# Kernel optimization log

Measured on AMD Instinct MI355X. Metric: run time of the kernel, lower is better.

The kernel has to match this reference:

```python
import jax, jax.numpy as jnp
import numpy as np

NUM_HEADS = 12


def setup_inputs() -> dict:
    key = jax.random.key(0)
    ks = jax.random.split(key, 8)
    B, Nq, Nk, C = 4, 2048, 2048, 768
    s = 0.02
    return {
        "query": jax.random.normal(ks[0], (B, Nq, C), dtype=jnp.float32),
        "key": jax.random.normal(ks[1], (B, Nk, C), dtype=jnp.float32),
        "value": jax.random.normal(ks[2], (B, Nk, C), dtype=jnp.float32),
        "Wq": jax.random.normal(ks[3], (C, C), dtype=jnp.float32) * s,
        "Wk": jax.random.normal(ks[4], (C, C), dtype=jnp.float32) * s,
        "Wv": jax.random.normal(ks[5], (C, C), dtype=jnp.float32) * s,
        "Wo": jax.random.normal(ks[6], (C, C), dtype=jnp.float32) * s,
        "bo": jnp.zeros((C,), dtype=jnp.float32),
    }


def reference(query, key, value, Wq, Wk, Wv, Wo, bo):
    B, Nq, C = query.shape
    Nk = key.shape[1]
    H = NUM_HEADS
    Dh = C // H
    scale = Dh ** -0.5
    # nn.Linear: x @ W.T ; split heads -> [B, H, N, Dh]
    q = (query @ Wq.T).reshape(B, Nq, H, Dh).transpose(0, 2, 1, 3)
    k = (key @ Wk.T).reshape(B, Nk, H, Dh).transpose(0, 2, 1, 3)
    v = (value @ Wv.T).reshape(B, Nk, H, Dh).transpose(0, 2, 1, 3)
    # attention logits [B, H, Nq, Nk]
    attn = jnp.einsum("bhqd,bhkd->bhqk", q, k) * scale
    attn = jax.nn.softmax(attn, axis=-1)
    x = jnp.einsum("bhqk,bhkd->bhqd", attn, v)  # [B, H, Nq, Dh]
    x = x.transpose(0, 2, 1, 3).reshape(B, Nq, C)
    return x @ Wo.T + bo
```

## Files before the change

### kernel.cpp

```cpp
#include <hip/hip_runtime.h>
#include <hip/hip_bf16.h>
#include <stdint.h>

typedef unsigned short u16;
typedef unsigned int   u32;
typedef unsigned long long u64;

typedef __attribute__((ext_vector_type(8)))  short short8;
typedef __attribute__((ext_vector_type(4)))  u32   u32x4;
typedef __attribute__((ext_vector_type(4)))  float f32x4;
typedef __attribute__((ext_vector_type(16))) float f32x16;


__device__ __forceinline__ u16 f2bf(float f) {
  u32 u = __builtin_bit_cast(u32, f);
  u += 0x7FFFu + ((u >> 16) & 1u);
  return (u16)(u >> 16);
}

__device__ __forceinline__ void gload16(const void* g, void* l) {
  __builtin_amdgcn_global_load_lds((__attribute__((address_space(1))) void*)(g),
                                   (__attribute__((address_space(3))) void*)(l),
                                   16, 0, 0);
}

__device__ __forceinline__ u32 cvtpk(float lo, float hi) {
  u32 r;
  asm("v_cvt_pk_bf16_f32 %0, %1, %2" : "=v"(r) : "v"(lo), "v"(hi));
  return r;
}


__global__ __launch_bounds__(256)
void cvt3_kernel(const float* __restrict__ a, const float* __restrict__ b,
                 const float* __restrict__ c, u16* __restrict__ oa,
                 u16* __restrict__ ob, u16* __restrict__ oc, int n4) {
  int i = blockIdx.x * 256 + threadIdx.x;
  if (i >= n4) return;
  const float* in = blockIdx.y == 0 ? a : blockIdx.y == 1 ? b : c;
  u16* out = blockIdx.y == 0 ? oa : blockIdx.y == 1 ? ob : oc;
  float4 v = reinterpret_cast<const float4*>(in)[i];
  u64 pk = (u64)f2bf(v.x) | ((u64)f2bf(v.y) << 16)
         | ((u64)f2bf(v.z) << 32) | ((u64)f2bf(v.w) << 48);
  reinterpret_cast<u64*>(out)[i] = pk;
}

__global__ __launch_bounds__(256)
void cvtw_kernel(const float* __restrict__ Wq, const float* __restrict__ Wk,
                 const float* __restrict__ Wv, const float* __restrict__ Wo,
                 u16* __restrict__ Wcat, u16* __restrict__ WoB, int n4, float qs) {
  int i = blockIdx.x * 256 + threadIdx.x;
  if (i >= n4) return;
  int y = blockIdx.y;
  const float* in = y == 0 ? Wq : y == 1 ? Wk : y == 2 ? Wv : Wo;
  u16* out = y == 0 ? Wcat : y == 1 ? (Wcat + 589824) : y == 2 ? (Wcat + 1179648) : WoB;
  float s = y == 0 ? qs : 1.f;
  float4 v = reinterpret_cast<const float4*>(in)[i];
  u64 pk = (u64)f2bf(v.x * s) | ((u64)f2bf(v.y * s) << 16)
         | ((u64)f2bf(v.z * s) << 32) | ((u64)f2bf(v.w * s) << 48);
  reinterpret_cast<u64*>(out)[i] = pk;
}

template<int MODE>
__global__ __launch_bounds__(256)
void gemm128(const u16* __restrict__ Aq, const u16* __restrict__ Ak,
             const u16* __restrict__ Av, const u16* __restrict__ Bw,
             u16* __restrict__ Cqk, u16* __restrict__ Vt,
             float* __restrict__ Cout, const float* __restrict__ bias) {
  constexpr int K  = 768;
  constexpr int KT = K / 32;
  constexpr int NBN = (MODE == 0) ? 18 : 6;
  __shared__ char lds[32768];
  char* A0 = lds;          char* A1 = lds + 8192;
  char* B0 = lds + 16384;  char* B1 = lds + 24576;

  const int tid = threadIdx.x, lane = tid & 63, wid = tid >> 6;
  const int hw = blockIdx.x;
  const int L = (hw & 7) * (64 * NBN / 8) + (hw >> 3);
  const int bm = L / NBN, bn = L - bm * NBN;
  const int wr = wid >> 1, wc = wid & 1;

  const u16* Abase = Aq;
  if constexpr (MODE == 0) Abase = (bn < 6) ? Aq : (bn < 12) ? Ak : Av;

  const char* Ag = (const char*)Abase + (size_t)bm * 128 * (K * 2);
  const char* Bg = (const char*)Bw    + (size_t)bn * 128 * (K * 2);

  f32x4 acc[4][4];
  #pragma unroll
  for (int m = 0; m < 4; ++m)
    #pragma unroll
    for (int n = 0; n < 4; ++n)
      #pragma unroll
      for (int r = 0; r < 4; ++r) acc[m][n][r] = 0.f;

  #pragma unroll
  for (int c = 0; c < 2; ++c) {
    int chunk = c * 4 + wid;
    int off = chunk * 1024 + lane * 16;
    int row = off >> 6, colb = off & 63;
    gload16(Ag + (size_t)row * (K * 2) + colb, A0 + chunk * 1024);
    gload16(Bg + (size_t)row * (K * 2) + colb, B0 + chunk * 1024);
  }
  __syncthreads();

  for (int kt = 0; kt < KT; ++kt) {
    const int cur = kt & 1;
    char* Ac = cur ? A1 : A0;  char* Bc = cur ? B1 : B0;
    char* An = cur ? A0 : A1;  char* Bn = cur ? B0 : B1;
    if (kt + 1 < KT) {
      #pragma unroll
      for (int c = 0; c < 2; ++c) {
        int chunk = c * 4 + wid;
        int off = chunk * 1024 + lane * 16;
        int row = off >> 6, colb = off & 63;
        gload16(Ag + (size_t)row * (K * 2) + (kt + 1) * 64 + colb, An + chunk * 1024);
        gload16(Bg + (size_t)row * (K * 2) + (kt + 1) * 64 + colb, Bn + chunk * 1024);
      }
    }
    short8 af[4], bf[4];
    #pragma unroll
    for (int m = 0; m < 4; ++m) {
      int row = wr * 64 + m * 16 + (lane & 15);
      af[m] = *reinterpret_cast<const short8*>(Ac + row * 64 + ((lane >> 4) * 16));
    }
    #pragma unroll
    for (int n = 0; n < 4; ++n) {
      int row = wc * 64 + n * 16 + (lane & 15);
      bf[n] = *reinterpret_cast<const short8*>(Bc + row * 64 + ((lane >> 4) * 16));
    }
    #pragma unroll
    for (int m = 0; m < 4; ++m)
      #pragma unroll
      for (int n = 0; n < 4; ++n)
        acc[m][n] = __builtin_amdgcn_mfma_f32_16x16x32_bf16(af[m], bf[n], acc[m][n], 0, 0, 0);
    __syncthreads();
  }

  if constexpr (MODE == 0) {
    if (bn < 12) {
      #pragma unroll
      for (int m = 0; m < 4; ++m) {
        int grow0 = bm * 128 + wr * 64 + m * 16 + ((lane >> 4) << 2);
        #pragma unroll
        for (int n = 0; n < 4; ++n) {
          int col = bn * 128 + wc * 64 + n * 16 + (lane & 15);
          #pragma unroll
          for (int r = 0; r < 4; ++r)
            Cqk[(size_t)(grow0 + r) * 1536 + col] = f2bf(acc[m][n][r]);
        }
      }
    } else {
      #pragma unroll
      for (int m = 0; m < 4; ++m) {
        int grow0 = bm * 128 + wr * 64 + m * 16 + ((lane >> 4) << 2);
        int bb = grow0 >> 11, nn = grow0 & 2047;
        #pragma unroll
        for (int n = 0; n < 4; ++n) {
          int vc = (bn - 12) * 128 + wc * 64 + n * 16 + (lane & 15);
          int hid = vc >> 6, d = vc & 63;
          u64 pk = (u64)f2bf(acc[m][n][0]) | ((u64)f2bf(acc[m][n][1]) << 16)
                 | ((u64)f2bf(acc[m][n][2]) << 32) | ((u64)f2bf(acc[m][n][3]) << 48);
          *reinterpret_cast<u64*>(Vt + ((size_t)(bb * 12 + hid) * 64 + d) * 2048 + nn) = pk;
        }
      }
    }
  } else {
    #pragma unroll
    for (int m = 0; m < 4; ++m) {
      int grow0 = bm * 128 + wr * 64 + m * 16 + ((lane >> 4) << 2);
      #pragma unroll
      for (int n = 0; n < 4; ++n) {
        int col = bn * 128 + wc * 64 + n * 16 + (lane & 15);
        float bs = bias[col];
        #pragma unroll
        for (int r = 0; r < 4; ++r)
          Cout[(size_t)(grow0 + r) * 768 + col] = acc[m][n][r] + bs;
      }
    }
  }
}

__global__ __launch_bounds__(256)
void attn_fwd(const u16* __restrict__ QK, const u16* __restrict__ Vt,
              u16* __restrict__ X) {
  __shared__ char lds[32768];
  char* K0 = lds;          char* K1 = lds + 8192;
  char* V0 = lds + 16384;  char* V1 = lds + 24576;

  const int tid = threadIdx.x, lane = tid & 63, wid = tid >> 6;
  const int hw = blockIdx.x;
  const int L = (hw & 7) * 96 + (hw >> 3);
  const int bh = L >> 4, qt = L & 15;
  const int b = bh / 12, h = bh - b * 12;
  const int hh = lane >> 5;

  const char* Qg = (const char*)QK + ((size_t)(b * 2048 + qt * 128) * 1536 + h * 64) * 2;
  const char* Kg = (const char*)QK + ((size_t)(b * 2048) * 1536 + 768 + h * 64) * 2;
  const char* Vg = (const char*)Vt + ((size_t)bh * 64 * 2048) * 2;

  const int off0 = wid * 1024 + lane * 16;
  const int off1 = off0 + 4096;
  const int r0 = off0 >> 7, i0 = (off0 & 127) ^ ((r0 & 7) << 4);
  const int r1 = off1 >> 7, i1 = (off1 & 127) ^ ((r1 & 7) << 4);
  const int pb0 = (r0 >> 2) & 7, pb1 = (r1 >> 2) & 7;
  const int kr0 = (r0 & 32) | ((((pb0 & 1) << 1) | ((pb0 >> 1) & 1) | (pb0 & 4)) << 2) | (r0 & 3);
  const int kr1 = (r1 & 32) | ((((pb1 & 1) << 1) | ((pb1 >> 1) & 1) | (pb1 & 4)) << 2) | (r1 & 3);
  const size_t kso0 = (size_t)kr0 * 3072 + i0, kso1 = (size_t)kr1 * 3072 + i1;
  const size_t vso0 = (size_t)r0 * 4096 + i0, vso1 = (size_t)r1 * 4096 + i1;

  gload16(Kg + kso0, K0 + off0);
  gload16(Kg + kso1, K0 + off1);
  gload16(Vg + vso0, V0 + off0);
  gload16(Vg + vso1, V0 + off1);

  short8 qf[4];
  {
    const char* Qrow = Qg + (size_t)(wid * 32 + (lane & 31)) * 3072 + hh * 16;
    #pragma unroll
    for (int kk = 0; kk < 4; ++kk)
      qf[kk] = *reinterpret_cast<const short8*>(Qrow + kk * 32);
  }
  __syncthreads();

  f32x16 o0, o1;
  #pragma unroll
  for (int r = 0; r < 16; ++r) { o0[r] = 0.f; o1[r] = 0.f; }
  float l_run = 0.f;

  for (int t = 0; t < 32; ++t) {
    const int cur = t & 1;
    char* Kc = cur ? K1 : K0;  char* Vc = cur ? V1 : V0;
    char* Kn = cur ? K0 : K1;  char* Vn = cur ? V0 : V1;
    if (t + 1 < 32) {
      const char* Kgn = Kg + (size_t)(t + 1) * 64 * 3072;
      const char* Vgn = Vg + (size_t)(t + 1) * 128;
      gload16(Kgn + kso0, Kn + off0);
      gload16(Kgn + kso1, Kn + off1);
      gload16(Vgn + vso0, Vn + off0);
      gload16(Vgn + vso1, Vn + off1);
    }

    f32x16 sa, sb;
    #pragma unroll
    for (int r = 0; r < 16; ++r) { sa[r] = 0.f; sb[r] = 0.f; }
    {
      const int ra = lane & 31;
      const int swa = (ra & 7) << 4;
      const char* Ka = Kc + ra * 128;
      const char* Kb2 = Kc + (32 + ra) * 128;
      __builtin_amdgcn_s_setprio(1);
      #pragma unroll
      for (int kk = 0; kk < 4; ++kk) {
        int inner = (kk * 32 + hh * 16) ^ swa;
        short8 ka = *reinterpret_cast<const short8*>(Ka + inner);
        short8 kb = *reinterpret_cast<const short8*>(Kb2 + inner);
        sa = __builtin_amdgcn_mfma_f32_32x32x16_bf16(ka, qf[kk], sa, 0, 0, 0);
        sb = __builtin_amdgcn_mfma_f32_32x32x16_bf16(kb, qf[kk], sb, 0, 0, 0);
      }
      __builtin_amdgcn_s_setprio(0);
    }

    float pa[16], pb[16];
    float s0 = 0.f, s1 = 0.f, s2 = 0.f, s3 = 0.f;
    #pragma unroll
    for (int r = 0; r < 16; r += 4) {
      pa[r]     = __builtin_amdgcn_exp2f(sa[r]);     s0 += pa[r];
      pa[r + 1] = __builtin_amdgcn_exp2f(sa[r + 1]); s1 += pa[r + 1];
      pa[r + 2] = __builtin_amdgcn_exp2f(sa[r + 2]); s2 += pa[r + 2];
      pa[r + 3] = __builtin_amdgcn_exp2f(sa[r + 3]); s3 += pa[r + 3];
    }
    #pragma unroll
    for (int r = 0; r < 16; r += 4) {
      pb[r]     = __builtin_amdgcn_exp2f(sb[r]);     s0 += pb[r];
      pb[r + 1] = __builtin_amdgcn_exp2f(sb[r + 1]); s1 += pb[r + 1];
      pb[r + 2] = __builtin_amdgcn_exp2f(sb[r + 2]); s2 += pb[r + 2];
      pb[r + 3] = __builtin_amdgcn_exp2f(sb[r + 3]); s3 += pb[r + 3];
    }
    l_run += (s0 + s1) + (s2 + s3);

    short8 pf[4];
    {
      u32x4 w0 = { cvtpk(pa[0],  pa[1]),  cvtpk(pa[2],  pa[3]),
                   cvtpk(pa[4],  pa[5]),  cvtpk(pa[6],  pa[7]) };
      u32x4 w1 = { cvtpk(pa[8],  pa[9]),  cvtpk(pa[10], pa[11]),
                   cvtpk(pa[12], pa[13]), cvtpk(pa[14], pa[15]) };
      u32x4 w2 = { cvtpk(pb[0],  pb[1]),  cvtpk(pb[2],  pb[3]),
                   cvtpk(pb[4],  pb[5]),  cvtpk(pb[6],  pb[7]) };
      u32x4 w3 = { cvtpk(pb[8],  pb[9]),  cvtpk(pb[10], pb[11]),
                   cvtpk(pb[12], pb[13]), cvtpk(pb[14], pb[15]) };
      pf[0] = __builtin_bit_cast(short8, w0);
      pf[1] = __builtin_bit_cast(short8, w1);
      pf[2] = __builtin_bit_cast(short8, w2);
      pf[3] = __builtin_bit_cast(short8, w3);
    }

    {
      const int rv = lane & 31;
      const int swv = (rv & 7) << 4;
      const char* Va = Vc + rv * 128;
      const char* Vb = Vc + (32 + rv) * 128;
      __builtin_amdgcn_s_setprio(1);
      #pragma unroll
      for (int st = 0; st < 4; ++st) {
        int inner = (st * 32 + hh * 16) ^ swv;
        short8 v0 = *reinterpret_cast<const short8*>(Va + inner);
        short8 v1 = *reinterpret_cast<const short8*>(Vb + inner);
        o0 = __builtin_amdgcn_mfma_f32_32x32x16_bf16(v0, pf[st], o0, 0, 0, 0);
        o1 = __builtin_amdgcn_mfma_f32_32x32x16_bf16(v1, pf[st], o1, 0, 0, 0);
      }
      __builtin_amdgcn_s_setprio(0);
    }
    __syncthreads();
  }

  l_run += __shfl_xor(l_run, 32);

  const float invl = __builtin_amdgcn_rcpf(l_run);
  const int q = qt * 128 + wid * 32 + (lane & 31);
  u16* Xp = X + (size_t)(b * 2048 + q) * 768;
  #pragma unroll
  for (int mt = 0; mt < 2; ++mt) {
    #pragma unroll
    for (int rr = 0; rr < 4; ++rr) {
      float e0 = (mt ? o1[rr * 4 + 0] : o0[rr * 4 + 0]) * invl;
      float e1 = (mt ? o1[rr * 4 + 1] : o0[rr * 4 + 1]) * invl;
      float e2 = (mt ? o1[rr * 4 + 2] : o0[rr * 4 + 2]) * invl;
      float e3 = (mt ? o1[rr * 4 + 3] : o0[rr * 4 + 3]) * invl;
      int col = h * 64 + mt * 32 + 8 * rr + 4 * hh;
      u64 pk = (u64)f2bf(e0) | ((u64)f2bf(e1) << 16)
             | ((u64)f2bf(e2) << 32) | ((u64)f2bf(e3) << 48);
      *reinterpret_cast<u64*>(Xp + col) = pk;
    }
  }
}


extern "C" void kernel_launch(void* const* d_in, const int* in_sizes, int n_in,
                              void* d_out, int out_size, void* d_ws, size_t ws_size,
                              hipStream_t stream) {
  const float* query = (const float*)d_in[0];
  const float* key   = (const float*)d_in[1];
  const float* value = (const float*)d_in[2];
  const float* Wq    = (const float*)d_in[3];
  const float* Wk    = (const float*)d_in[4];
  const float* Wv    = (const float*)d_in[5];
  const float* Wo    = (const float*)d_in[6];
  const float* bo    = (const float*)d_in[7];

  char* ws = (char*)d_ws;
  u16* Wcat = (u16*)ws;
  u16* WoB  = (u16*)(ws + (size_t)2304 * 768 * 2);
  u16* Xq   = (u16*)(ws + (size_t)2304 * 768 * 2 + (size_t)768 * 768 * 2);
  u16* Xk   = Xq  + (size_t)8192 * 768;
  u16* Xv   = Xk  + (size_t)8192 * 768;
  u16* QKb  = Xv  + (size_t)8192 * 768;
  u16* VtB  = QKb + (size_t)8192 * 1536;

  const float qs = 0.125f * 1.4426950408889634f;
  cvtw_kernel<<<dim3(576, 4), 256, 0, stream>>>(Wq, Wk, Wv, Wo, Wcat, WoB, 147456, qs);
  cvt3_kernel<<<dim3(6144, 3), 256, 0, stream>>>(query, key, value, Xq, Xk, Xv, 1572864);

  gemm128<0><<<dim3(1152), 256, 0, stream>>>(Xq, Xk, Xv, Wcat, QKb, VtB, nullptr, nullptr);
  attn_fwd<<<dim3(768), 256, 0, stream>>>(QKb, VtB, Xq);
  gemm128<1><<<dim3(384), 256, 0, stream>>>(Xq, nullptr, nullptr, WoB, nullptr, nullptr,
                                            (float*)d_out, bo);
}
```

Before: 169.8 us.

## Triple-buffer K/V tiles in attention with prefetch distance two

Moves the attention kernel's K/V staging from double to triple buffering in LDS, issuing global-to-LDS loads two tiles ahead. Full __syncthreads is replaced by explicit vmcnt waits plus s_barrier, so a wave only waits for the oldest outstanding tile. The aim is to hide more global load latency behind MFMA work, at the cost of 48KB of LDS per block, which may reduce occupancy.

```diff
diff --git a/kernel.cpp b/kernel.cpp
--- a/kernel.cpp
+++ b/kernel.cpp
@@ -184,9 +184,9 @@
 __global__ __launch_bounds__(256)
 void attn_fwd(const u16* __restrict__ QK, const u16* __restrict__ Vt,
               u16* __restrict__ X) {
-  __shared__ char lds[32768];
-  char* K0 = lds;          char* K1 = lds + 8192;
-  char* V0 = lds + 16384;  char* V1 = lds + 24576;
+  __shared__ char lds[49152];
+  char* Kb0 = lds;          char* Kb1 = lds + 8192;   char* Kb2 = lds + 16384;
+  char* Vb0 = lds + 24576;  char* Vb1 = lds + 32768;  char* Vb2 = lds + 40960;
 
   const int tid = threadIdx.x, lane = tid & 63, wid = tid >> 6;
   const int hw = blockIdx.x;
@@ -209,10 +209,17 @@
   const size_t kso0 = (size_t)kr0 * 3072 + i0, kso1 = (size_t)kr1 * 3072 + i1;
   const size_t vso0 = (size_t)r0 * 4096 + i0, vso1 = (size_t)r1 * 4096 + i1;
 
-  gload16(Kg + kso0, K0 + off0);
-  gload16(Kg + kso1, K0 + off1);
-  gload16(Vg + vso0, V0 + off0);
-  gload16(Vg + vso1, V0 + off1);
+  auto stage = [&](int t, char* Kd, char* Vd) {
+    const char* Kgn = Kg + (size_t)t * 64 * 3072;
+    const char* Vgn = Vg + (size_t)t * 128;
+    gload16(Kgn + kso0, Kd + off0);
+    gload16(Kgn + kso1, Kd + off1);
+    gload16(Vgn + vso0, Vd + off0);
+    gload16(Vgn + vso1, Vd + off1);
+  };
+
+  stage(0, Kb0, Vb0);
+  stage(1, Kb1, Vb1);
 
   short8 qf[4];
   {
@@ -221,26 +228,15 @@
     for (int kk = 0; kk < 4; ++kk)
       qf[kk] = *reinterpret_cast<const short8*>(Qrow + kk * 32);
   }
-  __syncthreads();
+  asm volatile("s_waitcnt vmcnt(8)" ::: "memory");
+  __builtin_amdgcn_s_barrier();
 
   f32x16 o0, o1;
   #pragma unroll
   for (int r = 0; r < 16; ++r) { o0[r] = 0.f; o1[r] = 0.f; }
   float l_run = 0.f;
 
-  for (int t = 0; t < 32; ++t) {
-    const int cur = t & 1;
-    char* Kc = cur ? K1 : K0;  char* Vc = cur ? V1 : V0;
-    char* Kn = cur ? K0 : K1;  char* Vn = cur ? V0 : V1;
-    if (t + 1 < 32) {
-      const char* Kgn = Kg + (size_t)(t + 1) * 64 * 3072;
-      const char* Vgn = Vg + (size_t)(t + 1) * 128;
-      gload16(Kgn + kso0, Kn + off0);
-      gload16(Kgn + kso1, Kn + off1);
-      gload16(Vgn + vso0, Vn + off0);
-      gload16(Vgn + vso1, Vn + off1);
-    }
-
+  auto tile_body = [&](const char* Kc, const char* Vc) {
     f32x16 sa, sb;
     #pragma unroll
     for (int r = 0; r < 16; ++r) { sa[r] = 0.f; sb[r] = 0.f; }
@@ -248,13 +244,13 @@
       const int ra = lane & 31;
       const int swa = (ra & 7) << 4;
       const char* Ka = Kc + ra * 128;
-      const char* Kb2 = Kc + (32 + ra) * 128;
+      const char* Kb_ = Kc + (32 + ra) * 128;
       __builtin_amdgcn_s_setprio(1);
       #pragma unroll
       for (int kk = 0; kk < 4; ++kk) {
         int inner = (kk * 32 + hh * 16) ^ swa;
         short8 ka = *reinterpret_cast<const short8*>(Ka + inner);
-        short8 kb = *reinterpret_cast<const short8*>(Kb2 + inner);
+        short8 kb = *reinterpret_cast<const short8*>(Kb_ + inner);
         sa = __builtin_amdgcn_mfma_f32_32x32x16_bf16(ka, qf[kk], sa, 0, 0, 0);
         sb = __builtin_amdgcn_mfma_f32_32x32x16_bf16(kb, qf[kk], sb, 0, 0, 0);
       }
@@ -299,20 +295,34 @@
       const int rv = lane & 31;
       const int swv = (rv & 7) << 4;
       const char* Va = Vc + rv * 128;
-      const char* Vb = Vc + (32 + rv) * 128;
+      const char* Vb_ = Vc + (32 + rv) * 128;
       __builtin_amdgcn_s_setprio(1);
       #pragma unroll
       for (int st = 0; st < 4; ++st) {
         int inner = (st * 32 + hh * 16) ^ swv;
         short8 v0 = *reinterpret_cast<const short8*>(Va + inner);
-        short8 v1 = *reinterpret_cast<const short8*>(Vb + inner);
+        short8 v1 = *reinterpret_cast<const short8*>(Vb_ + inner);
         o0 = __builtin_amdgcn_mfma_f32_32x32x16_bf16(v0, pf[st], o0, 0, 0, 0);
         o1 = __builtin_amdgcn_mfma_f32_32x32x16_bf16(v1, pf[st], o1, 0, 0, 0);
       }
       __builtin_amdgcn_s_setprio(0);
     }
-    __syncthreads();
-  }
+  };
+
+  char* Kc = Kb0; char* Kn1 = Kb1; char* Kn2 = Kb2;
+  char* Vc = Vb0; char* Vn1 = Vb1; char* Vn2 = Vb2;
+  for (int t = 0; t < 30; ++t) {
+    stage(t + 2, Kn2, Vn2);
+    tile_body(Kc, Vc);
+    asm volatile("s_waitcnt vmcnt(4)" ::: "memory");
+    __builtin_amdgcn_s_barrier();
+    char* tk = Kc; Kc = Kn1; Kn1 = Kn2; Kn2 = tk;
+    char* tv = Vc; Vc = Vn1; Vn1 = Vn2; Vn2 = tv;
+  }
+  tile_body(Kc, Vc);
+  asm volatile("s_waitcnt vmcnt(0)" ::: "memory");
+  __builtin_amdgcn_s_barrier();
+  tile_body(Kn1, Vn1);
 
   l_run += __shfl_xor(l_run, 32);
 
```

Result: no change. 171.6 us (+1.1%).

## Fuse fp32-to-bf16 activation conversion into QKV projection GEMM loads

Applied to the files above, without the earlier changes.

Removes the separate cvt3 conversion kernel and has the QKV GEMM stream fp32 query/key/value tiles directly into LDS with an XOR swizzle, converting to bf16 in registers before the MFMA. This drops one kernel launch and a full write and read of the bf16 activation copies. In exchange, the A tile doubles in LDS size (48KB for mode 0), doubles global A traffic per GEMM tile, and adds conversion instructions to the inner loop, which may reduce occupancy.

```diff
diff --git a/kernel.cpp b/kernel.cpp
--- a/kernel.cpp
+++ b/kernel.cpp
@@ -30,20 +30,6 @@
   return r;
 }
 
-
-__global__ __launch_bounds__(256)
-void cvt3_kernel(const float* __restrict__ a, const float* __restrict__ b,
-                 const float* __restrict__ c, u16* __restrict__ oa,
-                 u16* __restrict__ ob, u16* __restrict__ oc, int n4) {
-  int i = blockIdx.x * 256 + threadIdx.x;
-  if (i >= n4) return;
-  const float* in = blockIdx.y == 0 ? a : blockIdx.y == 1 ? b : c;
-  u16* out = blockIdx.y == 0 ? oa : blockIdx.y == 1 ? ob : oc;
-  float4 v = reinterpret_cast<const float4*>(in)[i];
-  u64 pk = (u64)f2bf(v.x) | ((u64)f2bf(v.y) << 16)
-         | ((u64)f2bf(v.z) << 32) | ((u64)f2bf(v.w) << 48);
-  reinterpret_cast<u64*>(out)[i] = pk;
-}
 
 __global__ __launch_bounds__(256)
 void cvtw_kernel(const float* __restrict__ Wq, const float* __restrict__ Wk,
@@ -63,16 +49,19 @@
 
 template<int MODE>
 __global__ __launch_bounds__(256)
-void gemm128(const u16* __restrict__ Aq, const u16* __restrict__ Ak,
-             const u16* __restrict__ Av, const u16* __restrict__ Bw,
+void gemm128(const float* __restrict__ Af0, const float* __restrict__ Af1,
+             const float* __restrict__ Af2, const u16* __restrict__ Ab,
+             const u16* __restrict__ Bw,
              u16* __restrict__ Cqk, u16* __restrict__ Vt,
              float* __restrict__ Cout, const float* __restrict__ bias) {
   constexpr int K  = 768;
   constexpr int KT = K / 32;
   constexpr int NBN = (MODE == 0) ? 18 : 6;
-  __shared__ char lds[32768];
-  char* A0 = lds;          char* A1 = lds + 8192;
-  char* B0 = lds + 16384;  char* B1 = lds + 24576;
+  __shared__ char lds[(MODE == 0) ? 49152 : 32768];
+  char* A0 = lds;
+  char* A1 = lds + ((MODE == 0) ? 16384 : 8192);
+  char* B0 = lds + ((MODE == 0) ? 32768 : 16384);
+  char* B1 = B0 + 8192;
 
   const int tid = threadIdx.x, lane = tid & 63, wid = tid >> 6;
   const int hw = blockIdx.x;
@@ -80,11 +69,15 @@
   const int bm = L / NBN, bn = L - bm * NBN;
   const int wr = wid >> 1, wc = wid & 1;
 
-  const u16* Abase = Aq;
-  if constexpr (MODE == 0) Abase = (bn < 6) ? Aq : (bn < 12) ? Ak : Av;
-
-  const char* Ag = (const char*)Abase + (size_t)bm * 128 * (K * 2);
-  const char* Bg = (const char*)Bw    + (size_t)bn * 128 * (K * 2);
+  const char* Agf = nullptr;
+  const char* Ag16 = nullptr;
+  if constexpr (MODE == 0) {
+    const float* Asrc = (bn < 6) ? Af0 : (bn < 12) ? Af1 : Af2;
+    Agf = (const char*)(Asrc + (size_t)bm * 128 * 768);
+  } else {
+    Ag16 = (const char*)Ab + (size_t)bm * 128 * (K * 2);
+  }
+  const char* Bg = (const char*)Bw + (size_t)bn * 128 * (K * 2);
 
   f32x4 acc[4][4];
   #pragma unroll
@@ -94,14 +87,39 @@
       #pragma unroll
       for (int r = 0; r < 4; ++r) acc[m][n][r] = 0.f;
 
-  #pragma unroll
-  for (int c = 0; c < 2; ++c) {
-    int chunk = c * 4 + wid;
-    int off = chunk * 1024 + lane * 16;
-    int row = off >> 6, colb = off & 63;
-    gload16(Ag + (size_t)row * (K * 2) + colb, A0 + chunk * 1024);
-    gload16(Bg + (size_t)row * (K * 2) + colb, B0 + chunk * 1024);
-  }
+  auto stageA32 = [&](char* An, int kt) {
+    if constexpr (MODE == 0) {
+      #pragma unroll
+      for (int j = 0; j < 4; ++j) {
+        int off = j * 4096 + wid * 1024 + lane * 16;
+        int row = off >> 7;
+        int isl = (off & 127) ^ ((row & 7) << 4);
+        gload16(Agf + (size_t)row * 3072 + kt * 128 + isl, An + off);
+      }
+    }
+  };
+  auto stageA16 = [&](char* An, int kt) {
+    if constexpr (MODE == 1) {
+      #pragma unroll
+      for (int c = 0; c < 2; ++c) {
+        int off = (c * 4 + wid) * 1024 + lane * 16;
+        int row = off >> 6, colb = off & 63;
+        gload16(Ag16 + (size_t)row * (K * 2) + kt * 64 + colb, An + off);
+      }
+    }
+  };
+  auto stageB = [&](char* Bn, int kt) {
+    #pragma unroll
+    for (int c = 0; c < 2; ++c) {
+      int off = (c * 4 + wid) * 1024 + lane * 16;
+      int row = off >> 6, colb = off & 63;
+      gload16(Bg + (size_t)row * (K * 2) + kt * 64 + colb, Bn + off);
+    }
+  };
+
+  stageA32(A0, 0);
+  stageA16(A0, 0);
+  stageB(B0, 0);
   __syncthreads();
 
   for (int kt = 0; kt < KT; ++kt) {
@@ -109,20 +127,26 @@
     char* Ac = cur ? A1 : A0;  char* Bc = cur ? B1 : B0;
     char* An = cur ? A0 : A1;  char* Bn = cur ? B0 : B1;
     if (kt + 1 < KT) {
-      #pragma unroll
-      for (int c = 0; c < 2; ++c) {
-        int chunk = c * 4 + wid;
-        int off = chunk * 1024 + lane * 16;
-        int row = off >> 6, colb = off & 63;
-        gload16(Ag + (size_t)row * (K * 2) + (kt + 1) * 64 + colb, An + chunk * 1024);
-        gload16(Bg + (size_t)row * (K * 2) + (kt + 1) * 64 + colb, Bn + chunk * 1024);
-      }
+      stageA32(An, kt + 1);
+      stageA16(An, kt + 1);
+      stageB(Bn, kt + 1);
     }
     short8 af[4], bf[4];
     #pragma unroll
     for (int m = 0; m < 4; ++m) {
       int row = wr * 64 + m * 16 + (lane & 15);
-      af[m] = *reinterpret_cast<const short8*>(Ac + row * 64 + ((lane >> 4) * 16));
+      if constexpr (MODE == 0) {
+        int swz = (row & 7) << 4;
+        int o1 = (lane >> 4) * 32;
+        const char* Ar = Ac + row * 128;
+        f32x4 lo = *reinterpret_cast<const f32x4*>(Ar + (o1 ^ swz));
+        f32x4 hi = *reinterpret_cast<const f32x4*>(Ar + ((o1 + 16) ^ swz));
+        u32x4 pk = { cvtpk(lo[0], lo[1]), cvtpk(lo[2], lo[3]),
+                     cvtpk(hi[0], hi[1]), cvtpk(hi[2], hi[3]) };
+        af[m] = __builtin_bit_cast(short8, pk);
+      } else {
+        af[m] = *reinterpret_cast<const short8*>(Ac + row * 64 + ((lane >> 4) * 16));
+      }
     }
     #pragma unroll
     for (int n = 0; n < 4; ++n) {
@@ -352,17 +376,15 @@
   u16* Wcat = (u16*)ws;
   u16* WoB  = (u16*)(ws + (size_t)2304 * 768 * 2);
   u16* Xq   = (u16*)(ws + (size_t)2304 * 768 * 2 + (size_t)768 * 768 * 2);
-  u16* Xk   = Xq  + (size_t)8192 * 768;
-  u16* Xv   = Xk  + (size_t)8192 * 768;
-  u16* QKb  = Xv  + (size_t)8192 * 768;
+  u16* QKb  = Xq  + (size_t)8192 * 768;
   u16* VtB  = QKb + (size_t)8192 * 1536;
 
   const float qs = 0.125f * 1.4426950408889634f;
   cvtw_kernel<<<dim3(576, 4), 256, 0, stream>>>(Wq, Wk, Wv, Wo, Wcat, WoB, 147456, qs);
-  cvt3_kernel<<<dim3(6144, 3), 256, 0, stream>>>(query, key, value, Xq, Xk, Xv, 1572864);
-
-  gemm128<0><<<dim3(1152), 256, 0, stream>>>(Xq, Xk, Xv, Wcat, QKb, VtB, nullptr, nullptr);
+
+  gemm128<0><<<dim3(1152), 256, 0, stream>>>(query, key, value, nullptr, Wcat,
+                                             QKb, VtB, nullptr, nullptr);
   attn_fwd<<<dim3(768), 256, 0, stream>>>(QKb, VtB, Xq);
-  gemm128<1><<<dim3(384), 256, 0, stream>>>(Xq, nullptr, nullptr, WoB, nullptr, nullptr,
-                                            (float*)d_out, bo);
-}
+  gemm128<1><<<dim3(384), 256, 0, stream>>>(nullptr, nullptr, nullptr, Xq, WoB,
+                                            nullptr, nullptr, (float*)d_out, bo);
+}
```

Result: faster. 161.2 us (median of 2 runs) (-5.1%).
